# Kernel tuning notes

Hardware: AMD Instinct MI355X
Metric: run time of the kernel (lower is better)

## Reference

```python
import jax, jax.numpy as jnp
import numpy as np

N_NODES = 100000
N_EDGES = 50000
NNZ = 800000
C = 256
EPS = 0.0  # fixed (train_eps=False)


def setup_inputs() -> dict:
    key = jax.random.key(0)
    k1, k2, k3, k4, k5 = jax.random.split(key, 5)
    x_0 = jax.random.normal(k1, (N_NODES, C), dtype=jnp.float32)
    node_idx = jax.random.randint(k2, (NNZ,), 0, N_NODES, dtype=jnp.int64 if jax.config.jax_enable_x64 else jnp.int32)
    edge_idx = jax.random.randint(k3, (NNZ,), 0, N_EDGES, dtype=jnp.int64 if jax.config.jax_enable_x64 else jnp.int32)
    W = jax.random.normal(k4, (C, C), dtype=jnp.float32) / np.sqrt(C)
    b = jax.random.normal(k5, (C,), dtype=jnp.float32) * 0.01
    return {"x_0": x_0, "node_idx": node_idx, "edge_idx": edge_idx, "W": W, "b": b}


def reference(x_0, node_idx, edge_idx, W, b):
    # vertex2edge: x_1 = B_1^T @ x_0  (each hyperedge sums its member nodes)
    x_1 = jax.ops.segment_sum(x_0[node_idx], edge_idx, num_segments=N_EDGES)  # (E, C)
    # edge2vertex: m_{1->0} = B_1 @ x_1  (each node sums its incident hyperedges)
    m_1_0 = jax.ops.segment_sum(x_1[edge_idx], node_idx, num_segments=N_NODES)  # (N, C)
    # GIN update: Theta @ ((1+eps) x_0 + m)
    x_0_out = ((1.0 + EPS) * x_0 + m_1_0) @ W.T + b
    # use_norm=False -> no row normalization
    return (x_0_out, x_1)
```

## Files before the change

kernel.cpp:

```cpp
#include <hip/hip_runtime.h>

#define N_NODES 100000
#define N_EDGES 50000
#define NNZ     800000
#define C       256

#define SHC_E 8
#define SHC_N 9
#define NBC_E ((N_EDGES + (1 << SHC_E) - 1) >> SHC_E)
#define NBC_N ((N_NODES + (1 << SHC_N) - 1) >> SHC_N)
#define CHUNK 4096
#define NCHUNK ((NNZ + CHUNK - 1) / CHUNK)

#define CONV_BLOCKS (N_NODES * C / 4 / 256)
#define PREPW_BLOCKS 32

typedef short  bf16x8 __attribute__((ext_vector_type(8)));
typedef float  f32x4  __attribute__((ext_vector_type(4)));

static __device__ __forceinline__ unsigned short f2bf(float f) {
    unsigned int u = __float_as_uint(f);
    u += 0x7FFF + ((u >> 16) & 1);
    return (unsigned short)(u >> 16);
}
static __device__ __forceinline__ float bf2f(unsigned short u) {
    return __uint_as_float(((unsigned int)u) << 16);
}


__global__ void convert_hist(const float* __restrict__ x0, unsigned short* __restrict__ x0b,
                             const int* __restrict__ node_idx, const int* __restrict__ edge_idx,
                             int* __restrict__ chunkhist_e, int* __restrict__ chunkhist_n,
                             const float* __restrict__ W, unsigned short* __restrict__ Wb) {
    int bid = blockIdx.x;
    if (bid < CONV_BLOCKS) {
        size_t i = (size_t)bid * 256 + threadIdx.x;
        float4 v = ((const float4*)x0)[i];
        ushort4 o;
        o.x = f2bf(v.x); o.y = f2bf(v.y); o.z = f2bf(v.z); o.w = f2bf(v.w);
        ((ushort4*)x0b)[i] = o;
    } else if (bid < CONV_BLOCKS + NCHUNK) {
        __shared__ int he[NBC_E], hn[NBC_N];
        const int tid = threadIdx.x;
        const int chunk = bid - CONV_BLOCKS;
        for (int i = tid; i < NBC_E; i += 256) he[i] = 0;
        for (int i = tid; i < NBC_N; i += 256) hn[i] = 0;
        __syncthreads();
        const int start = chunk * CHUNK;
        const int end = (start + CHUNK < NNZ) ? start + CHUNK : NNZ;
        for (int k = start + tid; k < end; k += 256) {
            atomicAdd(&he[edge_idx[k] >> SHC_E], 1);
            atomicAdd(&hn[node_idx[k] >> SHC_N], 1);
        }
        __syncthreads();
        for (int i = tid; i < NBC_E; i += 256) chunkhist_e[chunk * NBC_E + i] = he[i];
        for (int i = tid; i < NBC_N; i += 256) chunkhist_n[chunk * NBC_N + i] = hn[i];
    } else {
        int idx = (bid - CONV_BLOCKS - NCHUNK) * 256 + threadIdx.x;
        int h = idx >> 12, i = idx & 4095;
        int t = i >> 9, s = (i >> 6) & 7, l = i & 63;
        int m = l & 15, q = l >> 4;
        const float* src = W + (size_t)(h * 128 + 16 * t + m) * C + 32 * s + 8 * q;
        float4 f0 = *(const float4*)(src);
        float4 f1 = *(const float4*)(src + 4);
        unsigned short* d = Wb + (size_t)idx * 8;
        d[0] = f2bf(f0.x); d[1] = f2bf(f0.y); d[2] = f2bf(f0.z); d[3] = f2bf(f0.w);
        d[4] = f2bf(f1.x); d[5] = f2bf(f1.y); d[6] = f2bf(f1.z); d[7] = f2bf(f1.w);
    }
}


__global__ void coarse_scan(const int* __restrict__ chunkhist_e, const int* __restrict__ chunkhist_n,
                            int* __restrict__ gbase_e, int* __restrict__ gbase_n) {
    const int* ch = (blockIdx.x == 0) ? chunkhist_e : chunkhist_n;
    int* gbase = (blockIdx.x == 0) ? gbase_e : gbase_n;
    const int nb = (blockIdx.x == 0) ? NBC_E : NBC_N;
    int tid = threadIdx.x, lane = tid & 63, wid = tid >> 6;
    int v = 0;
    if (tid < nb)
        for (int c = 0; c < NCHUNK; c++) v += ch[c * nb + tid];
    int incl = v;
#pragma unroll
    for (int s = 1; s < 64; s <<= 1) { int u = __shfl_up(incl, s, 64); if (lane >= s) incl += u; }
    __shared__ int wsum[4];
    if (lane == 63) wsum[wid] = incl;
    __syncthreads();
    int add = 0;
    for (int i = 0; i < wid; i++) add += wsum[i];
    int excl = add + incl - v;
    if (tid <= nb) gbase[tid] = excl;
}


__global__ __launch_bounds__(256) void bin_coarse(const int* __restrict__ node_idx,
                                                  const int* __restrict__ edge_idx,
                                                  const int* __restrict__ gbase_e,
                                                  const int* __restrict__ gbase_n,
                                                  const int* __restrict__ chunkhist_e,
                                                  const int* __restrict__ chunkhist_n,
                                                  unsigned int* __restrict__ tmp_e,
                                                  unsigned int* __restrict__ tmp_n) {
    __shared__ int hist_e[NBC_E], hist_n[NBC_N];
    __shared__ int base_e[NBC_E], base_n[NBC_N];
    const int tid = threadIdx.x;
    const int chunk = blockIdx.x;
    const int start = chunk * CHUNK;
    const int end = (start + CHUNK < NNZ) ? start + CHUNK : NNZ;

    for (int i = tid; i < NBC_E; i += 256) {
        int pre = gbase_e[i];
        for (int c = 0; c < chunk; c++) pre += chunkhist_e[c * NBC_E + i];
        base_e[i] = pre;
        hist_e[i] = 0;
    }
    for (int i = tid; i < NBC_N; i += 256) {
        int pre = gbase_n[i];
        for (int c = 0; c < chunk; c++) pre += chunkhist_n[c * NBC_N + i];
        base_n[i] = pre;
        hist_n[i] = 0;
    }
    __syncthreads();

    for (int k = start + tid; k < end; k += 256) {
        int ni = node_idx[k], ei = edge_idx[k];
        int be = ei >> SHC_E;
        int pe = base_e[be] + atomicAdd(&hist_e[be], 1);
        tmp_e[pe] = ((unsigned int)ni << SHC_E) | (unsigned int)(ei & ((1 << SHC_E) - 1));
        int bn = ni >> SHC_N;
        int pn = base_n[bn] + atomicAdd(&hist_n[bn], 1);
        tmp_n[pn] = ((unsigned int)ei << SHC_N) | (unsigned int)(ni & ((1 << SHC_N) - 1));
    }
}


template <int SHC, int NTOT>
static __device__ __forceinline__ void scatter_fine_body(const unsigned int* __restrict__ tmp,
                                                         const int* __restrict__ gbase,
                                                         int* __restrict__ off,
                                                         int* __restrict__ perm,
                                                         int b, int* hist, int* cur, int* wsum) {
    constexpr int NK = 1 << SHC;
    const int tid = threadIdx.x, lane = tid & 63, wid = tid >> 6;
    const int start = gbase[b], end = gbase[b + 1];
    for (int t = tid; t < NK; t += 256) hist[t] = 0;
    __syncthreads();
    for (int k = start + tid; k < end; k += 256)
        atomicAdd(&hist[tmp[k] & (NK - 1)], 1);
    __syncthreads();
    int v0, v1 = 0, local;
    if constexpr (NK == 512) { v0 = hist[2 * tid]; v1 = hist[2 * tid + 1]; local = v0 + v1; }
    else                     { v0 = hist[tid]; local = v0; }
    int incl = local;
#pragma unroll
    for (int s = 1; s < 64; s <<= 1) { int u = __shfl_up(incl, s, 64); if (lane >= s) incl += u; }
    if (lane == 63) wsum[wid] = incl;
    __syncthreads();
    int add = 0;
    for (int i = 0; i < wid; i++) add += wsum[i];
    int base = start + add + incl - local;
    const int kbase = b << SHC;
    if constexpr (NK == 512) {
        int key0 = kbase + 2 * tid;
        if (key0 < NTOT)     off[key0] = base;
        if (key0 + 1 < NTOT) off[key0 + 1] = base + v0;
        cur[2 * tid]     = base;
        cur[2 * tid + 1] = base + v0;
    } else {
        int key0 = kbase + tid;
        if (key0 < NTOT) off[key0] = base;
        cur[tid] = base;
    }
    if (b == ((NTOT - 1) >> SHC) && tid == 0) off[NTOT] = end;
    __syncthreads();
    for (int k = start + tid; k < end; k += 256) {
        unsigned int u = tmp[k];
        int pos = atomicAdd(&cur[u & (NK - 1)], 1);
        perm[pos] = (int)(u >> SHC);
    }
}

__global__ __launch_bounds__(256) void scatter_fine(const unsigned int* __restrict__ tmp_e,
                                                    const unsigned int* __restrict__ tmp_n,
                                                    const int* __restrict__ gbase_e,
                                                    const int* __restrict__ gbase_n,
                                                    int* __restrict__ off_e, int* __restrict__ off_n,
                                                    int* __restrict__ perm_e, int* __restrict__ perm_n) {
    __shared__ int hist[1 << SHC_N], cur[1 << SHC_N], wsum[4];
    if (blockIdx.x < NBC_E)
        scatter_fine_body<SHC_E, N_EDGES>(tmp_e, gbase_e, off_e, perm_e, blockIdx.x, hist, cur, wsum);
    else
        scatter_fine_body<SHC_N, N_NODES>(tmp_n, gbase_n, off_n, perm_n, blockIdx.x - NBC_E, hist, cur, wsum);
}


__global__ void pull_edge(const unsigned short* __restrict__ x0b,
                          const int* __restrict__ off, const int* __restrict__ perm,
                          float* __restrict__ x1, unsigned short* __restrict__ x1b) {
    int e = blockIdx.x * 4 + (threadIdx.x >> 6);
    int lane = threadIdx.x & 63;
    int half = lane >> 5;
    int cl = lane & 31;
    int s0 = off[e], s1 = off[e + 1];
    float a[8] = {0, 0, 0, 0, 0, 0, 0, 0};
    float b[8] = {0, 0, 0, 0, 0, 0, 0, 0};
    int k = s0;
    for (; k + 16 <= s1; k += 16) {
        int r0 = perm[k + half],      r1 = perm[k + 2 + half];
        int r2 = perm[k + 4 + half],  r3 = perm[k + 6 + half];
        int r4 = perm[k + 8 + half],  r5 = perm[k + 10 + half];
        int r6 = perm[k + 12 + half], r7 = perm[k + 14 + half];
        bf16x8 u0 = *(const bf16x8*)(x0b + (size_t)r0 * C + cl * 8);
        bf16x8 u1 = *(const bf16x8*)(x0b + (size_t)r1 * C + cl * 8);
        bf16x8 u2 = *(const bf16x8*)(x0b + (size_t)r2 * C + cl * 8);
        bf16x8 u3 = *(const bf16x8*)(x0b + (size_t)r3 * C + cl * 8);
        bf16x8 u4 = *(const bf16x8*)(x0b + (size_t)r4 * C + cl * 8);
        bf16x8 u5 = *(const bf16x8*)(x0b + (size_t)r5 * C + cl * 8);
        bf16x8 u6 = *(const bf16x8*)(x0b + (size_t)r6 * C + cl * 8);
        bf16x8 u7 = *(const bf16x8*)(x0b + (size_t)r7 * C + cl * 8);
#pragma unroll
        for (int j = 0; j < 8; j++) {
            a[j] += bf2f((unsigned short)u0[j]); b[j] += bf2f((unsigned short)u1[j]);
            a[j] += bf2f((unsigned short)u2[j]); b[j] += bf2f((unsigned short)u3[j]);
            a[j] += bf2f((unsigned short)u4[j]); b[j] += bf2f((unsigned short)u5[j]);
            a[j] += bf2f((unsigned short)u6[j]); b[j] += bf2f((unsigned short)u7[j]);
        }
    }
    for (; k + 8 <= s1; k += 8) {
        int r0 = perm[k + half],     r1 = perm[k + 2 + half];
        int r2 = perm[k + 4 + half], r3 = perm[k + 6 + half];
        bf16x8 u0 = *(const bf16x8*)(x0b + (size_t)r0 * C + cl * 8);
        bf16x8 u1 = *(const bf16x8*)(x0b + (size_t)r1 * C + cl * 8);
        bf16x8 u2 = *(const bf16x8*)(x0b + (size_t)r2 * C + cl * 8);
        bf16x8 u3 = *(const bf16x8*)(x0b + (size_t)r3 * C + cl * 8);
#pragma unroll
        for (int j = 0; j < 8; j++) {
            a[j] += bf2f((unsigned short)u0[j]); b[j] += bf2f((unsigned short)u1[j]);
            a[j] += bf2f((unsigned short)u2[j]); b[j] += bf2f((unsigned short)u3[j]);
        }
    }
    for (; k + 2 <= s1; k += 2) {
        int r = perm[k + half];
        bf16x8 u = *(const bf16x8*)(x0b + (size_t)r * C + cl * 8);
#pragma unroll
        for (int j = 0; j < 8; j++) a[j] += bf2f((unsigned short)u[j]);
    }
    if (k < s1 && half == 0) {
        int r = perm[k];
        bf16x8 u = *(const bf16x8*)(x0b + (size_t)r * C + cl * 8);
#pragma unroll
        for (int j = 0; j < 8; j++) a[j] += bf2f((unsigned short)u[j]);
    }
#pragma unroll
    for (int j = 0; j < 8; j++) a[j] += b[j];
#pragma unroll
    for (int j = 0; j < 8; j++) a[j] += __shfl_down(a[j], 32);
    if (half == 0) {
        f32x4 vlo = {a[0], a[1], a[2], a[3]};
        f32x4 vhi = {a[4], a[5], a[6], a[7]};
        __builtin_nontemporal_store(vlo, (f32x4*)(x1 + (size_t)e * C + cl * 8));
        __builtin_nontemporal_store(vhi, (f32x4*)(x1 + (size_t)e * C + cl * 8 + 4));
        bf16x8 o;
#pragma unroll
        for (int j = 0; j < 8; j++) o[j] = (short)f2bf(a[j]);
        *(bf16x8*)(x1b + (size_t)e * C + cl * 8) = o;
    }
}

__global__ void pull_node(const unsigned short* __restrict__ x0b,
                          const unsigned short* __restrict__ x1b,
                          const int* __restrict__ off, const int* __restrict__ perm,
                          unsigned short* __restrict__ xm) {
    int n = blockIdx.x * 4 + (threadIdx.x >> 6);
    int lane = threadIdx.x & 63;
    int half = lane >> 5;
    int cl = lane & 31;
    int s0 = off[n], s1 = off[n + 1];
    float a[8] = {0, 0, 0, 0, 0, 0, 0, 0};
    float b[8] = {0, 0, 0, 0, 0, 0, 0, 0};
    int k = s0;
    for (; k + 8 <= s1; k += 8) {
        int r0 = perm[k + half],     r1 = perm[k + 2 + half];
        int r2 = perm[k + 4 + half], r3 = perm[k + 6 + half];
        bf16x8 u0 = *(const bf16x8*)(x1b + (size_t)r0 * C + cl * 8);
        bf16x8 u1 = *(const bf16x8*)(x1b + (size_t)r1 * C + cl * 8);
        bf16x8 u2 = *(const bf16x8*)(x1b + (size_t)r2 * C + cl * 8);
        bf16x8 u3 = *(const bf16x8*)(x1b + (size_t)r3 * C + cl * 8);
#pragma unroll
        for (int j = 0; j < 8; j++) {
            a[j] += bf2f((unsigned short)u0[j]); b[j] += bf2f((unsigned short)u1[j]);
            a[j] += bf2f((unsigned short)u2[j]); b[j] += bf2f((unsigned short)u3[j]);
        }
    }
    for (; k + 2 <= s1; k += 2) {
        int r = perm[k + half];
        bf16x8 u = *(const bf16x8*)(x1b + (size_t)r * C + cl * 8);
#pragma unroll
        for (int j = 0; j < 8; j++) a[j] += bf2f((unsigned short)u[j]);
    }
    if (k < s1 && half == 0) {
        int r = perm[k];
        bf16x8 u = *(const bf16x8*)(x1b + (size_t)r * C + cl * 8);
#pragma unroll
        for (int j = 0; j < 8; j++) a[j] += bf2f((unsigned short)u[j]);
    }
#pragma unroll
    for (int j = 0; j < 8; j++) a[j] += b[j];
#pragma unroll
    for (int j = 0; j < 8; j++) a[j] += __shfl_down(a[j], 32);
    if (half == 0) {
        bf16x8 xr = *(const bf16x8*)(x0b + (size_t)n * C + cl * 8);
        bf16x8 o;
#pragma unroll
        for (int j = 0; j < 8; j++) o[j] = (short)f2bf(a[j] + bf2f((unsigned short)xr[j]));
        *(bf16x8*)(xm + (size_t)n * C + cl * 8) = o;
    }
}


__global__ __launch_bounds__(512) void mfma_gemm3(const unsigned short* __restrict__ xm,
                                                  const unsigned short* __restrict__ Wb,
                                                  const float* __restrict__ bias,
                                                  float* __restrict__ out) {
    __shared__ unsigned short Bs[4096 * 8];
    const int rt = blockIdx.x;
    const int tid = threadIdx.x;
    const int w = tid >> 6, lane = tid & 63;
    const int m = lane & 15, q = lane >> 4;
    const int row = rt * 128 + w * 16 + m;
    const int arow = row < N_NODES ? row : N_NODES - 1;

    bf16x8 a[8];
    const unsigned short* ap = xm + (size_t)arow * C + q * 8;
#pragma unroll
    for (int s = 0; s < 8; s++) a[s] = *(const bf16x8*)(ap + 32 * s);

    const int r0 = rt * 128 + w * 16 + q * 4;

    for (int h = 0; h < 2; h++) {
        __syncthreads();
        const unsigned short* wsrc = Wb + (size_t)h * (4096 * 8);
#pragma unroll
        for (int it = 0; it < 8; it++) {
            int i = it * 512 + tid;
            *(bf16x8*)(Bs + (size_t)i * 8) = *(const bf16x8*)(wsrc + (size_t)i * 8);
        }
        __syncthreads();

        f32x4 acc[8];
#pragma unroll
        for (int t = 0; t < 8; t++) acc[t] = (f32x4){0.f, 0.f, 0.f, 0.f};
#pragma unroll
        for (int s = 0; s < 8; s++) {
#pragma unroll
            for (int t = 0; t < 8; t++) {
                bf16x8 b = *(const bf16x8*)(Bs + ((t * 8 + s) * 64 + lane) * 8);
                acc[t] = __builtin_amdgcn_mfma_f32_16x16x32_bf16(a[s], b, acc[t], 0, 0, 0);
            }
        }

        const int colbase = h * 128;
#pragma unroll
        for (int t = 0; t < 8; t++) {
            float bv = bias[colbase + t * 16 + m];
#pragma unroll
            for (int r = 0; r < 4; r++) {
                int rr = r0 + r;
                if (rr < N_NODES)
                    __builtin_nontemporal_store(acc[t][r] + bv,
                                                out + (size_t)rr * C + colbase + t * 16 + m);
            }
        }
    }
}


__global__ void init_kernel(const float* __restrict__ x0, float* __restrict__ out) {
    long long i = (long long)blockIdx.x * blockDim.x + threadIdx.x;
    const long long n_node4 = (long long)N_NODES * C / 4;
    const long long n_tot4  = (long long)(N_NODES + N_EDGES) * C / 4;
    float4* o4 = (float4*)out;
    if (i < n_node4)      o4[i] = ((const float4*)x0)[i];
    else if (i < n_tot4)  o4[i] = make_float4(0.f, 0.f, 0.f, 0.f);
}

__global__ void scatter_add_kernel(const float* __restrict__ src,
                                   const int* __restrict__ src_idx,
                                   const int* __restrict__ dst_idx,
                                   float* __restrict__ dst) {
    int j    = blockIdx.x * (blockDim.x >> 6) + (threadIdx.x >> 6);
    int lane = threadIdx.x & 63;
    if (j >= NNZ) return;
    int s = src_idx[j];
    int d = dst_idx[j];
    const float4 v = *(const float4*)(src + (long long)s * C + lane * 4);
    float* dp = dst + (long long)d * C + lane * 4;
    atomicAdd(dp + 0, v.x); atomicAdd(dp + 1, v.y);
    atomicAdd(dp + 2, v.z); atomicAdd(dp + 3, v.w);
}

__global__ void gin_gemm_kernel(const float* __restrict__ W,
                                const float* __restrict__ b,
                                float* __restrict__ out) {
    int n = blockIdx.x;
    int t = threadIdx.x;
    __shared__ float xs[C];
    float* row = out + (long long)n * C;
    xs[t] = row[t];
    __syncthreads();
    float acc = b[t];
    const float* wrow = W + t * C;
#pragma unroll 8
    for (int k = 0; k < C; k += 4) {
        float4 xv = *(const float4*)(xs + k);
        float4 wv = *(const float4*)(wrow + k);
        acc = fmaf(xv.x, wv.x, acc); acc = fmaf(xv.y, wv.y, acc);
        acc = fmaf(xv.z, wv.z, acc); acc = fmaf(xv.w, wv.w, acc);
    }
    row[t] = acc;
}


extern "C" void kernel_launch(void* const* d_in, const int* in_sizes, int n_in,
                              void* d_out, int out_size, void* d_ws, size_t ws_size,
                              hipStream_t stream) {
    const float* x0       = (const float*)d_in[0];
    const int*   node_idx = (const int*)d_in[1];
    const int*   edge_idx = (const int*)d_in[2];
    const float* W        = (const float*)d_in[3];
    const float* b        = (const float*)d_in[4];
    float* out = (float*)d_out;
    float* x1  = out + (size_t)N_NODES * C;

    char* p = (char*)d_ws;
    size_t used = 0;
    auto alloc = [&](size_t bytes) {
        char* r = p + used;
        used += (bytes + 255) & ~(size_t)255;
        return r;
    };
    int* off_e   = (int*)alloc((N_EDGES + 1) * 4);
    int* off_n   = (int*)alloc((N_NODES + 1) * 4);
    int* gbase_e = (int*)alloc((NBC_E + 1) * 4);
    int* gbase_n = (int*)alloc((NBC_N + 1) * 4);
    int* chunkhist_e = (int*)alloc((size_t)NCHUNK * NBC_E * 4);
    int* chunkhist_n = (int*)alloc((size_t)NCHUNK * NBC_N * 4);
    int* perm_e  = (int*)alloc((size_t)NNZ * 4);
    int* perm_n  = (int*)alloc((size_t)NNZ * 4);
    unsigned short* Wb  = (unsigned short*)alloc((size_t)2 * 4096 * 8 * 2);
    unsigned short* x0b = (unsigned short*)alloc((size_t)N_NODES * C * 2);
    unsigned short* x1b = (unsigned short*)alloc((size_t)N_EDGES * C * 2);
    unsigned short* xm  = (unsigned short*)alloc((size_t)N_NODES * C * 2);

    if (ws_size < used) {
        long long tot4 = (long long)(N_NODES + N_EDGES) * C / 4;
        init_kernel<<<(int)((tot4 + 255) / 256), 256, 0, stream>>>(x0, out);
        int grid = NNZ / 4;
        scatter_add_kernel<<<grid, 256, 0, stream>>>(x0, node_idx, edge_idx, x1);
        scatter_add_kernel<<<grid, 256, 0, stream>>>(x1, edge_idx, node_idx, out);
        gin_gemm_kernel<<<N_NODES, 256, 0, stream>>>(W, b, out);
        return;
    }

    convert_hist<<<CONV_BLOCKS + NCHUNK + PREPW_BLOCKS, 256, 0, stream>>>(
        x0, x0b, node_idx, edge_idx, chunkhist_e, chunkhist_n, W, Wb);

    coarse_scan<<<2, 256, 0, stream>>>(chunkhist_e, chunkhist_n, gbase_e, gbase_n);

    unsigned int* tmp_e = (unsigned int*)x1b;
    unsigned int* tmp_n = (unsigned int*)xm;
    bin_coarse<<<NCHUNK, 256, 0, stream>>>(node_idx, edge_idx, gbase_e, gbase_n,
                                           chunkhist_e, chunkhist_n, tmp_e, tmp_n);
    scatter_fine<<<NBC_E + NBC_N, 256, 0, stream>>>(tmp_e, tmp_n, gbase_e, gbase_n,
                                                    off_e, off_n, perm_e, perm_n);

    pull_edge<<<N_EDGES / 4, 256, 0, stream>>>(x0b, off_e, perm_e, x1, x1b);
    pull_node<<<N_NODES / 4, 256, 0, stream>>>(x0b, x1b, off_n, perm_n, xm);

    const int row_tiles = (N_NODES + 127) / 128;
    mfma_gemm3<<<row_tiles, 512, 0, stream>>>(xm, Wb, b, out);
}
```

Before: 480.6 us.

## Parallelize per-chunk prefix scan and split GEMM column halves across blocks

Adds a scan_chunks kernel that computes, for every coarse bin, an exclusive prefix over chunks. bin_coarse can then read its base offset directly instead of looping over all earlier chunks, which was quadratic work in the chunk index. The coarse scan now reads per-bin totals. Separately, the GEMM launches two blocks per row tile, one per 128-column half of W. This doubles the block count and removes the serial two-pass loop with its extra barriers, but each xm row tile is now read twice. An extra kernel launch is also added.

New measurement: 429.7 us. -10.6%, faster.

```diff
diff --git a/kernel.cpp b/kernel.cpp
--- a/kernel.cpp
+++ b/kernel.cpp
@@ -70,15 +70,36 @@
 }
 
 
-__global__ void coarse_scan(const int* __restrict__ chunkhist_e, const int* __restrict__ chunkhist_n,
+__global__ void scan_chunks(int* __restrict__ chunkhist_e, int* __restrict__ chunkhist_n,
+                            int* __restrict__ binsum_e, int* __restrict__ binsum_n) {
+    bool isE = blockIdx.x < NBC_E;
+    int* ch = isE ? chunkhist_e : chunkhist_n;
+    int* binsum = isE ? binsum_e : binsum_n;
+    const int nb = isE ? NBC_E : NBC_N;
+    const int bin = isE ? blockIdx.x : blockIdx.x - NBC_E;
+    int tid = threadIdx.x, lane = tid & 63, wid = tid >> 6;
+    int v = (tid < NCHUNK) ? ch[tid * nb + bin] : 0;
+    int incl = v;
+#pragma unroll
+    for (int s = 1; s < 64; s <<= 1) { int u = __shfl_up(incl, s, 64); if (lane >= s) incl += u; }
+    __shared__ int wsum[4];
+    if (lane == 63) wsum[wid] = incl;
+    __syncthreads();
+    int add = 0;
+    for (int i = 0; i < wid; i++) add += wsum[i];
+    int excl = add + incl - v;
+    if (tid < NCHUNK) ch[tid * nb + bin] = excl;
+    if (tid == NCHUNK - 1) binsum[bin] = excl + v;
+}
+
+
+__global__ void coarse_scan(const int* __restrict__ binsum_e, const int* __restrict__ binsum_n,
                             int* __restrict__ gbase_e, int* __restrict__ gbase_n) {
-    const int* ch = (blockIdx.x == 0) ? chunkhist_e : chunkhist_n;
+    const int* binsum = (blockIdx.x == 0) ? binsum_e : binsum_n;
     int* gbase = (blockIdx.x == 0) ? gbase_e : gbase_n;
     const int nb = (blockIdx.x == 0) ? NBC_E : NBC_N;
     int tid = threadIdx.x, lane = tid & 63, wid = tid >> 6;
-    int v = 0;
-    if (tid < nb)
-        for (int c = 0; c < NCHUNK; c++) v += ch[c * nb + tid];
+    int v = (tid < nb) ? binsum[tid] : 0;
     int incl = v;
 #pragma unroll
     for (int s = 1; s < 64; s <<= 1) { int u = __shfl_up(incl, s, 64); if (lane >= s) incl += u; }
@@ -108,15 +129,11 @@
     const int end = (start + CHUNK < NNZ) ? start + CHUNK : NNZ;
 
     for (int i = tid; i < NBC_E; i += 256) {
-        int pre = gbase_e[i];
-        for (int c = 0; c < chunk; c++) pre += chunkhist_e[c * NBC_E + i];
-        base_e[i] = pre;
+        base_e[i] = gbase_e[i] + chunkhist_e[chunk * NBC_E + i];
         hist_e[i] = 0;
     }
     for (int i = tid; i < NBC_N; i += 256) {
-        int pre = gbase_n[i];
-        for (int c = 0; c < chunk; c++) pre += chunkhist_n[c * NBC_N + i];
-        base_n[i] = pre;
+        base_n[i] = gbase_n[i] + chunkhist_n[chunk * NBC_N + i];
         hist_n[i] = 0;
     }
     __syncthreads();
@@ -317,13 +334,22 @@
 }
 
 
-__global__ __launch_bounds__(512) void mfma_gemm3(const unsigned short* __restrict__ xm,
+__global__ __launch_bounds__(512) void mfma_gemm2(const unsigned short* __restrict__ xm,
                                                   const unsigned short* __restrict__ Wb,
                                                   const float* __restrict__ bias,
                                                   float* __restrict__ out) {
-    __shared__ unsigned short Bs[4096 * 8];
-    const int rt = blockIdx.x;
+    __shared__ unsigned short Bs[8 * 8 * 64 * 8];
+    const int rt = blockIdx.x >> 1;
+    const int colbase = (blockIdx.x & 1) * 128;
     const int tid = threadIdx.x;
+
+    const unsigned short* wsrc = Wb + (size_t)(blockIdx.x & 1) * (4096 * 8);
+#pragma unroll
+    for (int it = 0; it < 8; it++) {
+        int i = it * 512 + tid;
+        *(bf16x8*)(Bs + (size_t)i * 8) = *(const bf16x8*)(wsrc + (size_t)i * 8);
+    }
+
     const int w = tid >> 6, lane = tid & 63;
     const int m = lane & 15, q = lane >> 4;
     const int row = rt * 128 + w * 16 + m;
@@ -334,41 +360,31 @@
 #pragma unroll
     for (int s = 0; s < 8; s++) a[s] = *(const bf16x8*)(ap + 32 * s);
 
+    __syncthreads();
+
+    f32x4 acc[8];
+#pragma unroll
+    for (int t = 0; t < 8; t++) acc[t] = (f32x4){0.f, 0.f, 0.f, 0.f};
+
+#pragma unroll
+    for (int s = 0; s < 8; s++) {
+#pragma unroll
+        for (int t = 0; t < 8; t++) {
+            bf16x8 b = *(const bf16x8*)(Bs + ((t * 8 + s) * 64 + lane) * 8);
+            acc[t] = __builtin_amdgcn_mfma_f32_16x16x32_bf16(a[s], b, acc[t], 0, 0, 0);
+        }
+    }
+
     const int r0 = rt * 128 + w * 16 + q * 4;
-
-    for (int h = 0; h < 2; h++) {
-        __syncthreads();
-        const unsigned short* wsrc = Wb + (size_t)h * (4096 * 8);
-#pragma unroll
-        for (int it = 0; it < 8; it++) {
-            int i = it * 512 + tid;
-            *(bf16x8*)(Bs + (size_t)i * 8) = *(const bf16x8*)(wsrc + (size_t)i * 8);
-        }
-        __syncthreads();
-
-        f32x4 acc[8];
-#pragma unroll
-        for (int t = 0; t < 8; t++) acc[t] = (f32x4){0.f, 0.f, 0.f, 0.f};
-#pragma unroll
-        for (int s = 0; s < 8; s++) {
-#pragma unroll
-            for (int t = 0; t < 8; t++) {
-                bf16x8 b = *(const bf16x8*)(Bs + ((t * 8 + s) * 64 + lane) * 8);
-                acc[t] = __builtin_amdgcn_mfma_f32_16x16x32_bf16(a[s], b, acc[t], 0, 0, 0);
-            }
-        }
-
-        const int colbase = h * 128;
-#pragma unroll
-        for (int t = 0; t < 8; t++) {
-            float bv = bias[colbase + t * 16 + m];
-#pragma unroll
-            for (int r = 0; r < 4; r++) {
-                int rr = r0 + r;
-                if (rr < N_NODES)
-                    __builtin_nontemporal_store(acc[t][r] + bv,
-                                                out + (size_t)rr * C + colbase + t * 16 + m);
-            }
+#pragma unroll
+    for (int t = 0; t < 8; t++) {
+        float bv = bias[colbase + t * 16 + m];
+#pragma unroll
+        for (int r = 0; r < 4; r++) {
+            int rr = r0 + r;
+            if (rr < N_NODES)
+                __builtin_nontemporal_store(acc[t][r] + bv,
+                                            out + (size_t)rr * C + colbase + t * 16 + m);
         }
     }
 }
@@ -442,6 +458,8 @@
     int* off_n   = (int*)alloc((N_NODES + 1) * 4);
     int* gbase_e = (int*)alloc((NBC_E + 1) * 4);
     int* gbase_n = (int*)alloc((NBC_N + 1) * 4);
+    int* binsum_e = (int*)alloc(NBC_E * 4);
+    int* binsum_n = (int*)alloc(NBC_N * 4);
     int* chunkhist_e = (int*)alloc((size_t)NCHUNK * NBC_E * 4);
     int* chunkhist_n = (int*)alloc((size_t)NCHUNK * NBC_N * 4);
     int* perm_e  = (int*)alloc((size_t)NNZ * 4);
@@ -464,7 +482,9 @@
     convert_hist<<<CONV_BLOCKS + NCHUNK + PREPW_BLOCKS, 256, 0, stream>>>(
         x0, x0b, node_idx, edge_idx, chunkhist_e, chunkhist_n, W, Wb);
 
-    coarse_scan<<<2, 256, 0, stream>>>(chunkhist_e, chunkhist_n, gbase_e, gbase_n);
+    scan_chunks<<<NBC_E + NBC_N, 256, 0, stream>>>(chunkhist_e, chunkhist_n, binsum_e, binsum_n);
+
+    coarse_scan<<<2, 256, 0, stream>>>(binsum_e, binsum_n, gbase_e, gbase_n);
 
     unsigned int* tmp_e = (unsigned int*)x1b;
     unsigned int* tmp_n = (unsigned int*)xm;
@@ -477,5 +497,5 @@
     pull_node<<<N_NODES / 4, 256, 0, stream>>>(x0b, x1b, off_n, perm_n, xm);
 
     const int row_tiles = (N_NODES + 127) / 128;
-    mfma_gemm3<<<row_tiles, 512, 0, stream>>>(xm, Wb, b, out);
-}
+    mfma_gemm2<<<row_tiles * 2, 512, 0, stream>>>(xm, Wb, b, out);
+}
```
